# Kernel tuning notes

Hardware: AMD Instinct MI355X
Metric: run time of the kernel (lower is better)

Reference implementation:

```python
import jax, jax.numpy as jnp
import numpy as np

TAU = 0.07        # temperature from init_kwargs
EPS = 1e-8        # torch F.cosine_similarity eps
NEG_INF = -1e9    # mask fill value used by the original module


def setup_inputs() -> dict:
    key = jax.random.key(0)
    k1, k2 = jax.random.split(key)
    B, D = 4096, 512
    anchor = jax.random.normal(k1, (B, D), dtype=jnp.float32)
    positive = jax.random.normal(k2, (B, D), dtype=jnp.float32)
    return {"anchor": anchor, "positive": positive}


def reference(anchor, positive):
    B = anchor.shape[0]
    N = 2 * B
    emb = jnp.concatenate([anchor, positive], axis=0)          # (2B, D)
    # cosine similarity matrix == normalized dot products (same math as the
    # broadcasted F.cosine_similarity, without the O(N^2 D) intermediate)
    norm = jnp.maximum(jnp.linalg.norm(emb, axis=1, keepdims=True), EPS)
    z = emb / norm
    sim = jnp.matmul(z, z.T) / TAU                             # (2B, 2B)

    idx = jnp.arange(N)
    pos_idx = (idx + B) % N                                    # positive pair index
    pos_logits = sim[idx, pos_idx][:, None]                    # (2B, 1)

    # negatives: everything except self and the positive pair
    neg_mask = (
        jnp.ones((N, N), dtype=bool)
        .at[idx, idx].set(False)
        .at[idx, pos_idx].set(False)
    )
    neg_logits = jnp.where(neg_mask, sim, NEG_INF)             # (2B, 2B)

    all_logits = jnp.concatenate([pos_logits, neg_logits], axis=1)  # (2B, 2B+1)
    loss_per_sample = -pos_logits[:, 0] + jax.scipy.special.logsumexp(all_logits, axis=1)
    # every row has a positive, so valid_samples is all-True; reduction='mean'
    return loss_per_sample.mean()
```

## Files before the change

### kernel.cpp

```cpp
#include <hip/hip_runtime.h>
#include <hip/hip_bf16.h>
#include <stdint.h>


#define N_TOT   8192
#define B_HALF  4096
#define DDIM    512
#define INV_TAU 14.285714285714286f

typedef __bf16 bf16x8 __attribute__((ext_vector_type(8)));
typedef __bf16 bf16x4 __attribute__((ext_vector_type(4)));
typedef float  floatx4 __attribute__((ext_vector_type(4)));

__device__ __forceinline__ void gl2lds16(const void* g, void* l) {
    __builtin_amdgcn_global_load_lds(
        (const __attribute__((address_space(1))) void*)g,
        (__attribute__((address_space(3))) void*)l, 16, 0, 0);
}

__global__ __launch_bounds__(256) void knorm(const float* __restrict__ anchor,
                                             const float* __restrict__ positive,
                                             __bf16* __restrict__ z,
                                             float* __restrict__ row_sums,
                                             float* __restrict__ out) {
    const int row  = blockIdx.x * 4 + (threadIdx.x >> 6);
    const int lane = threadIdx.x & 63;
    if (lane == 0) row_sums[row] = 0.0f;
    if (blockIdx.x == 0 && threadIdx.x == 0) out[0] = 0.0f;
    const float* src = (row < B_HALF) ? (anchor + (size_t)row * DDIM)
                                      : (positive + (size_t)(row - B_HALF) * DDIM);
    float4 v0 = ((const float4*)src)[lane];
    float4 v1 = ((const float4*)src)[lane + 64];
    float ss = v0.x*v0.x + v0.y*v0.y + v0.z*v0.z + v0.w*v0.w
             + v1.x*v1.x + v1.y*v1.y + v1.z*v1.z + v1.w*v1.w;
    #pragma unroll
    for (int m = 1; m < 64; m <<= 1) ss += __shfl_xor(ss, m, 64);
    const float inv = 1.0f / fmaxf(sqrtf(ss), 1e-8f);
    bf16x4 o0, o1;
    o0[0] = (__bf16)(v0.x*inv); o0[1] = (__bf16)(v0.y*inv);
    o0[2] = (__bf16)(v0.z*inv); o0[3] = (__bf16)(v0.w*inv);
    o1[0] = (__bf16)(v1.x*inv); o1[1] = (__bf16)(v1.y*inv);
    o1[2] = (__bf16)(v1.z*inv); o1[3] = (__bf16)(v1.w*inv);
    bf16x4* dst = (bf16x4*)(z + (size_t)row * DDIM);
    dst[lane]      = o0;
    dst[lane + 64] = o1;
}

__global__ __launch_bounds__(256) void ksim(const __bf16* __restrict__ z,
                                            float* __restrict__ row_sums,
                                            float* __restrict__ pos_sims) {
    const int bid = (int)blockIdx.x;
    const int xcd = bid & 7, l = bid >> 3;
    const int pr  = xcd + 8 * (l / 65);
    const int j   = l % 65;
    int rt, ct;
    if (j <= pr) { rt = j;          ct = pr;      }
    else         { rt = j - pr - 1; ct = 63 - pr; }
    const bool diag = (rt == ct);
    const bool posb = (ct == rt + 32);

    const int r0 = rt * 128, c0 = ct * 128;
    const int tid  = threadIdx.x;
    const int w    = tid >> 6, lane = tid & 63;
    const int quad = lane >> 4, nlo = lane & 15;
    const int wrow = (w >> 1) * 64, wcol = (w & 1) * 64;

    __shared__ __align__(16) char smem[32768];
    char* As = smem;
    char* Bs = smem + 16384;
    const char* Bbase = diag ? As : Bs;

    floatx4 acc[4][4];
    #pragma unroll
    for (int a = 0; a < 4; a++)
        #pragma unroll
        for (int b = 0; b < 4; b++) acc[a][b] = (floatx4){0.f, 0.f, 0.f, 0.f};

    const int srow = lane >> 3;
    const int p    = lane & 7;

    for (int kb = 0; kb < DDIM; kb += 64) {
        #pragma unroll
        for (int it = 0; it < 4; it++) {
            const int c  = w * 4 + it;
            const int rr = c * 8 + srow;
            const int lc = (p - rr) & 7;
            gl2lds16(z + (size_t)(r0 + rr) * DDIM + kb + lc * 8, As + c * 1024);
            if (!diag)
                gl2lds16(z + (size_t)(c0 + rr) * DDIM + kb + lc * 8, Bs + c * 1024);
        }
        __syncthreads();

        #pragma unroll
        for (int ks = 0; ks < 2; ks++) {
            bf16x8 af[4], bfr[4];
            #pragma unroll
            for (int mi = 0; mi < 4; mi++) {
                const int rr = wrow + mi * 16 + nlo;
                const int pc = (ks * 4 + quad + rr) & 7;
                af[mi] = *(const bf16x8*)(As + rr * 128 + pc * 16);
            }
            #pragma unroll
            for (int ni = 0; ni < 4; ni++) {
                const int rr = wcol + ni * 16 + nlo;
                const int pc = (ks * 4 + quad + rr) & 7;
                bfr[ni] = *(const bf16x8*)(Bbase + rr * 128 + pc * 16);
            }
            #pragma unroll
            for (int mi = 0; mi < 4; mi++)
                #pragma unroll
                for (int ni = 0; ni < 4; ni++)
                    acc[mi][ni] = __builtin_amdgcn_mfma_f32_16x16x32_bf16(
                        af[mi], bfr[ni], acc[mi][ni], 0, 0, 0);
        }
        __syncthreads();
    }

    if (diag) {
        #pragma unroll
        for (int mi = 0; mi < 4; mi++) {
            #pragma unroll
            for (int reg = 0; reg < 4; reg++) {
                const int i = r0 + wrow + mi * 16 + quad * 4 + reg;
                float rs = 0.f;
                #pragma unroll
                for (int ni = 0; ni < 4; ni++) {
                    const int j2 = c0 + wcol + ni * 16 + nlo;
                    const float e = __expf(acc[mi][ni][reg] * INV_TAU - INV_TAU);
                    rs += (j2 == i) ? 0.f : e;
                }
                rs += __shfl_xor(rs, 1, 64);
                rs += __shfl_xor(rs, 2, 64);
                rs += __shfl_xor(rs, 4, 64);
                rs += __shfl_xor(rs, 8, 64);
                if (nlo == 0) atomicAdd(&row_sums[i], rs);
            }
        }
    } else {
        float cs[4] = {0.f, 0.f, 0.f, 0.f};
        #pragma unroll
        for (int mi = 0; mi < 4; mi++) {
            #pragma unroll
            for (int reg = 0; reg < 4; reg++) {
                const int i = r0 + wrow + mi * 16 + quad * 4 + reg;
                const int ipos = i ^ B_HALF;
                float rs = 0.f;
                #pragma unroll
                for (int ni = 0; ni < 4; ni++) {
                    const int j2 = c0 + wcol + ni * 16 + nlo;
                    const float sim = acc[mi][ni][reg] * INV_TAU;
                    const float e = __expf(sim - INV_TAU);
                    if (posb && j2 == ipos) {
                        pos_sims[i]  = sim;
                        pos_sims[j2] = sim;
                    }
                    rs += e;
                    cs[ni] += e;
                }
                rs += __shfl_xor(rs, 1, 64);
                rs += __shfl_xor(rs, 2, 64);
                rs += __shfl_xor(rs, 4, 64);
                rs += __shfl_xor(rs, 8, 64);
                if (nlo == 0) atomicAdd(&row_sums[i], rs);
            }
        }
        #pragma unroll
        for (int ni = 0; ni < 4; ni++) {
            float c = cs[ni];
            c += __shfl_xor(c, 16, 64);
            c += __shfl_xor(c, 32, 64);
            if (quad == 0)
                atomicAdd(&row_sums[c0 + wcol + ni * 16 + nlo], c);
        }
    }
}

__global__ __launch_bounds__(256) void kfinal(const float* __restrict__ row_sums,
                                              const float* __restrict__ pos_sims,
                                              float* __restrict__ out) {
    const int r = blockIdx.x * 256 + threadIdx.x;
    float v = INV_TAU + __logf(row_sums[r]) - pos_sims[r];
    #pragma unroll
    for (int m = 1; m < 64; m <<= 1) v += __shfl_xor(v, m, 64);
    __shared__ float wsum[4];
    if ((threadIdx.x & 63) == 0) wsum[threadIdx.x >> 6] = v;
    __syncthreads();
    if (threadIdx.x == 0)
        atomicAdd(out, (wsum[0] + wsum[1] + wsum[2] + wsum[3]) * (1.0f / (float)N_TOT));
}

extern "C" void kernel_launch(void* const* d_in, const int* in_sizes, int n_in,
                              void* d_out, int out_size, void* d_ws, size_t ws_size,
                              hipStream_t stream) {
    const float* anchor   = (const float*)d_in[0];
    const float* positive = (const float*)d_in[1];
    float* out = (float*)d_out;

    char* ws = (char*)d_ws;
    __bf16* z        = (__bf16*)ws;
    float*  row_sums = (float*)(ws + 8388608);
    float*  pos_sims = (float*)(ws + 8388608 + 32768);

    knorm<<<N_TOT / 4, 256, 0, stream>>>(anchor, positive, z, row_sums, out);
    ksim<<<2080, 256, 0, stream>>>(z, row_sums, pos_sims);
    kfinal<<<N_TOT / 256, 256, 0, stream>>>(row_sums, pos_sims, out);
}
```

Measured before the change: 132.3 us.

## Enlarge similarity tiles to 256x256 with double-buffered LDS and block-level row reductions

The similarity kernel moves from 128x128 tiles on 256 threads to 256x256 tiles on 1024 threads (16 waves), so each loaded row of z is reused across more outputs. Global-to-LDS loads now go into two alternating buffers, letting the next K-slice load while MFMAs run on the current one. Row and column exp-sums are first combined in shared memory, then written with one atomic per row or column instead of one per wave. The cost is 128 KB of LDS per block (one block per CU) and only 528 blocks, which is just over two waves on the device and may leave a poorly filled tail.

Result: faster. 123.5 us (-6.6%).

```diff
diff --git a/kernel.cpp b/kernel.cpp
--- a/kernel.cpp
+++ b/kernel.cpp
@@ -46,29 +46,28 @@
     dst[lane + 64] = o1;
 }
 
-__global__ __launch_bounds__(256) void ksim(const __bf16* __restrict__ z,
-                                            float* __restrict__ row_sums,
-                                            float* __restrict__ pos_sims) {
+__global__ __launch_bounds__(1024, 4) void ksim(const __bf16* __restrict__ z,
+                                                float* __restrict__ row_sums,
+                                                float* __restrict__ pos_sims) {
     const int bid = (int)blockIdx.x;
     const int xcd = bid & 7, l = bid >> 3;
-    const int pr  = xcd + 8 * (l / 65);
-    const int j   = l % 65;
+    const int pr  = xcd + 8 * (l / 33);
+    const int j   = l % 33;
     int rt, ct;
     if (j <= pr) { rt = j;          ct = pr;      }
-    else         { rt = j - pr - 1; ct = 63 - pr; }
+    else         { rt = j - pr - 1; ct = 31 - pr; }
     const bool diag = (rt == ct);
-    const bool posb = (ct == rt + 32);
-
-    const int r0 = rt * 128, c0 = ct * 128;
+    const bool posb = (ct == rt + 16);
+
+    const int r0 = rt * 256, c0 = ct * 256;
     const int tid  = threadIdx.x;
     const int w    = tid >> 6, lane = tid & 63;
     const int quad = lane >> 4, nlo = lane & 15;
-    const int wrow = (w >> 1) * 64, wcol = (w & 1) * 64;
-
-    __shared__ __align__(16) char smem[32768];
-    char* As = smem;
-    char* Bs = smem + 16384;
-    const char* Bbase = diag ? As : Bs;
+    const int wr   = w >> 2,   wc  = w & 3;
+    const int wrow = wr * 64,  wcol = wc * 64;
+
+    __shared__ __align__(16) char A0[32768], B0[32768];
+    __shared__ __align__(16) char A1[32768], B1[32768];
 
     floatx4 acc[4][4];
     #pragma unroll
@@ -79,100 +78,112 @@
     const int srow = lane >> 3;
     const int p    = lane & 7;
 
-    for (int kb = 0; kb < DDIM; kb += 64) {
+#define STG_A(dst, KB) do {                                                     \
+        _Pragma("unroll") for (int it = 0; it < 2; it++) {                      \
+            const int c  = w * 2 + it;                                          \
+            const int rr = c * 8 + srow;                                        \
+            const int lc = (p - rr) & 7;                                        \
+            gl2lds16(z + (size_t)(r0 + rr) * DDIM + (KB) + lc * 8,              \
+                     (dst) + c * 1024);                                         \
+        } } while (0)
+#define STG_B(dst, KB) do {                                                     \
+        _Pragma("unroll") for (int it = 0; it < 2; it++) {                      \
+            const int c  = w * 2 + it;                                          \
+            const int rr = c * 8 + srow;                                        \
+            const int lc = (p - rr) & 7;                                        \
+            gl2lds16(z + (size_t)(c0 + rr) * DDIM + (KB) + lc * 8,              \
+                     (dst) + c * 1024);                                         \
+        } } while (0)
+
+#define KSTEP(CA, CB, NA, NB, KB_NEXT, DO_STAGE) do {                           \
+        if (DO_STAGE) { STG_A(NA, KB_NEXT); if (!diag) STG_B(NB, KB_NEXT); }    \
+        const char* Bb_ = diag ? (CA) : (CB);                                   \
+        _Pragma("unroll") for (int ks = 0; ks < 2; ks++) {                      \
+            bf16x8 af[4], bfr[4];                                               \
+            _Pragma("unroll") for (int mi = 0; mi < 4; mi++) {                  \
+                const int rr = wrow + mi * 16 + nlo;                            \
+                const int pc = (ks * 4 + quad + rr) & 7;                        \
+                af[mi] = *(const bf16x8*)((CA) + rr * 128 + pc * 16);           \
+            }                                                                   \
+            _Pragma("unroll") for (int ni = 0; ni < 4; ni++) {                  \
+                const int rr = wcol + ni * 16 + nlo;                            \
+                const int pc = (ks * 4 + quad + rr) & 7;                        \
+                bfr[ni] = *(const bf16x8*)(Bb_ + rr * 128 + pc * 16);           \
+            }                                                                   \
+            _Pragma("unroll") for (int mi = 0; mi < 4; mi++)                    \
+                _Pragma("unroll") for (int ni = 0; ni < 4; ni++)                \
+                    acc[mi][ni] = __builtin_amdgcn_mfma_f32_16x16x32_bf16(      \
+                        af[mi], bfr[ni], acc[mi][ni], 0, 0, 0);                 \
+        }                                                                       \
+        __syncthreads();                                                        \
+    } while (0)
+
+    STG_A(A0, 0); if (!diag) STG_B(B0, 0);
+    __syncthreads();
+
+    KSTEP(A0, B0, A1, B1,  64, 1);
+    KSTEP(A1, B1, A0, B0, 128, 1);
+    KSTEP(A0, B0, A1, B1, 192, 1);
+    KSTEP(A1, B1, A0, B0, 256, 1);
+    KSTEP(A0, B0, A1, B1, 320, 1);
+    KSTEP(A1, B1, A0, B0, 384, 1);
+    KSTEP(A0, B0, A1, B1, 448, 1);
+    KSTEP(A1, B1, A0, B0,   0, 0);
+
+    float* rbuf = (float*)A0;
+    float* cbuf = (float*)(A0 + 4096);
+
+    float cs[4] = {0.f, 0.f, 0.f, 0.f};
+    #pragma unroll
+    for (int mi = 0; mi < 4; mi++) {
         #pragma unroll
-        for (int it = 0; it < 4; it++) {
-            const int c  = w * 4 + it;
-            const int rr = c * 8 + srow;
-            const int lc = (p - rr) & 7;
-            gl2lds16(z + (size_t)(r0 + rr) * DDIM + kb + lc * 8, As + c * 1024);
-            if (!diag)
-                gl2lds16(z + (size_t)(c0 + rr) * DDIM + kb + lc * 8, Bs + c * 1024);
-        }
-        __syncthreads();
-
-        #pragma unroll
-        for (int ks = 0; ks < 2; ks++) {
-            bf16x8 af[4], bfr[4];
-            #pragma unroll
-            for (int mi = 0; mi < 4; mi++) {
-                const int rr = wrow + mi * 16 + nlo;
-                const int pc = (ks * 4 + quad + rr) & 7;
-                af[mi] = *(const bf16x8*)(As + rr * 128 + pc * 16);
-            }
+        for (int reg = 0; reg < 4; reg++) {
+            const int il = wrow + mi * 16 + quad * 4 + reg;
+            const int i  = r0 + il;
+            const int ipos = i ^ B_HALF;
+            float rs = 0.f;
             #pragma unroll
             for (int ni = 0; ni < 4; ni++) {
-                const int rr = wcol + ni * 16 + nlo;
-                const int pc = (ks * 4 + quad + rr) & 7;
-                bfr[ni] = *(const bf16x8*)(Bbase + rr * 128 + pc * 16);
+                const int j2 = c0 + wcol + ni * 16 + nlo;
+                const float sim = acc[mi][ni][reg] * INV_TAU;
+                float e = __expf(sim - INV_TAU);
+                if (diag && j2 == i) e = 0.f;
+                if (posb && j2 == ipos) {
+                    pos_sims[i]  = sim;
+                    pos_sims[j2] = sim;
+                }
+                rs += e;
+                cs[ni] += e;
             }
-            #pragma unroll
-            for (int mi = 0; mi < 4; mi++)
-                #pragma unroll
-                for (int ni = 0; ni < 4; ni++)
-                    acc[mi][ni] = __builtin_amdgcn_mfma_f32_16x16x32_bf16(
-                        af[mi], bfr[ni], acc[mi][ni], 0, 0, 0);
+            rs += __shfl_xor(rs, 1, 64);
+            rs += __shfl_xor(rs, 2, 64);
+            rs += __shfl_xor(rs, 4, 64);
+            rs += __shfl_xor(rs, 8, 64);
+            if (nlo == 0) rbuf[il * 4 + wc] = rs;
         }
-        __syncthreads();
     }
-
-    if (diag) {
-        #pragma unroll
-        for (int mi = 0; mi < 4; mi++) {
-            #pragma unroll
-            for (int reg = 0; reg < 4; reg++) {
-                const int i = r0 + wrow + mi * 16 + quad * 4 + reg;
-                float rs = 0.f;
-                #pragma unroll
-                for (int ni = 0; ni < 4; ni++) {
-                    const int j2 = c0 + wcol + ni * 16 + nlo;
-                    const float e = __expf(acc[mi][ni][reg] * INV_TAU - INV_TAU);
-                    rs += (j2 == i) ? 0.f : e;
-                }
-                rs += __shfl_xor(rs, 1, 64);
-                rs += __shfl_xor(rs, 2, 64);
-                rs += __shfl_xor(rs, 4, 64);
-                rs += __shfl_xor(rs, 8, 64);
-                if (nlo == 0) atomicAdd(&row_sums[i], rs);
-            }
-        }
-    } else {
-        float cs[4] = {0.f, 0.f, 0.f, 0.f};
-        #pragma unroll
-        for (int mi = 0; mi < 4; mi++) {
-            #pragma unroll
-            for (int reg = 0; reg < 4; reg++) {
-                const int i = r0 + wrow + mi * 16 + quad * 4 + reg;
-                const int ipos = i ^ B_HALF;
-                float rs = 0.f;
-                #pragma unroll
-                for (int ni = 0; ni < 4; ni++) {
-                    const int j2 = c0 + wcol + ni * 16 + nlo;
-                    const float sim = acc[mi][ni][reg] * INV_TAU;
-                    const float e = __expf(sim - INV_TAU);
-                    if (posb && j2 == ipos) {
-                        pos_sims[i]  = sim;
-                        pos_sims[j2] = sim;
-                    }
-                    rs += e;
-                    cs[ni] += e;
-                }
-                rs += __shfl_xor(rs, 1, 64);
-                rs += __shfl_xor(rs, 2, 64);
-                rs += __shfl_xor(rs, 4, 64);
-                rs += __shfl_xor(rs, 8, 64);
-                if (nlo == 0) atomicAdd(&row_sums[i], rs);
-            }
-        }
+    if (!diag) {
         #pragma unroll
         for (int ni = 0; ni < 4; ni++) {
             float c = cs[ni];
             c += __shfl_xor(c, 16, 64);
             c += __shfl_xor(c, 32, 64);
-            if (quad == 0)
-                atomicAdd(&row_sums[c0 + wcol + ni * 16 + nlo], c);
+            if (quad == 0) cbuf[(wcol + ni * 16 + nlo) * 4 + wr] = c;
         }
     }
+    __syncthreads();
+    if (tid < 256) {
+        const float s = rbuf[tid * 4] + rbuf[tid * 4 + 1]
+                      + rbuf[tid * 4 + 2] + rbuf[tid * 4 + 3];
+        atomicAdd(&row_sums[r0 + tid], s);
+    } else if (tid < 512 && !diag) {
+        const int c = tid - 256;
+        atomicAdd(&row_sums[c0 + c], cbuf[c * 4] + cbuf[c * 4 + 1]
+                                   + cbuf[c * 4 + 2] + cbuf[c * 4 + 3]);
+    }
+#undef KSTEP
+#undef STG_A
+#undef STG_B
 }
 
 __global__ __launch_bounds__(256) void kfinal(const float* __restrict__ row_sums,
@@ -202,6 +213,6 @@
     float*  pos_sims = (float*)(ws + 8388608 + 32768);
 
     knorm<<<N_TOT / 4, 256, 0, stream>>>(anchor, positive, z, row_sums, out);
-    ksim<<<2080, 256, 0, stream>>>(z, row_sums, pos_sims);
+    ksim<<<528, 1024, 0, stream>>>(z, row_sums, pos_sims);
     kfinal<<<N_TOT / 256, 256, 0, stream>>>(row_sums, pos_sims, out);
 }
```
